# Kernel tuning notes

Hardware: AMD Instinct MI355X
Metric: run time of the kernel (lower is better)

## Reference

```python
import jax, jax.numpy as jnp
import numpy as np

NUM_NODES = 20000
HIDDEN = 64
NUM_EDGES = 640000
LEAK = 0.2  # PyG GATConv negative_slope default


def gat_conv(x, w, a_src, a_dst, b, src, dst, n):
    # x: [N, F_in]; w: [F_in, H*C]; a_src/a_dst: [H, C]; edges j=src -> i=dst
    H, C = a_src.shape
    xe = (x @ w).reshape(n, H, C)                         # [N, H, C]
    es = jnp.einsum('nhc,hc->nh', xe, a_src)              # alpha_src per node
    ed = jnp.einsum('nhc,hc->nh', xe, a_dst)              # alpha_dst per node
    e = jax.nn.leaky_relu(es[src] + ed[dst], LEAK)        # [E, H] edge logits
    # segment softmax over each destination's incoming edges
    m = jax.ops.segment_max(e, dst, num_segments=n)
    p = jnp.exp(e - m[dst])
    s = jax.ops.segment_sum(p, dst, num_segments=n)
    alpha = p / s[dst]                                    # [E, H]
    out = jax.ops.segment_sum(alpha[:, :, None] * xe[src], dst, num_segments=n)
    return out.reshape(n, H * C) + b                      # concat heads + bias


def setup_inputs() -> dict:
    key = jax.random.key(0)
    ks = jax.random.split(key, 16)
    B, S, N, Hd = 4, 12, NUM_NODES, HIDDEN
    sc = 0.1
    inp = {}
    inp['x'] = jax.random.normal(ks[0], (B, S, N), jnp.float32)
    inp['edge_index'] = jax.random.randint(ks[1], (2, NUM_EDGES), 0, N, jnp.int32)
    inp['proj_w'] = jax.random.normal(ks[2], (S, Hd), jnp.float32) * sc
    inp['proj_b'] = jnp.zeros((Hd,), jnp.float32)
    inp['gat0_w'] = jax.random.normal(ks[3], (Hd, Hd), jnp.float32) * sc
    inp['gat0_asrc'] = jax.random.normal(ks[4], (8, 8), jnp.float32) * sc
    inp['gat0_adst'] = jax.random.normal(ks[5], (8, 8), jnp.float32) * sc
    inp['gat0_b'] = jnp.zeros((Hd,), jnp.float32)
    inp['gat1_w'] = jax.random.normal(ks[6], (Hd, Hd), jnp.float32) * sc
    inp['gat1_asrc'] = jax.random.normal(ks[7], (8, 8), jnp.float32) * sc
    inp['gat1_adst'] = jax.random.normal(ks[8], (8, 8), jnp.float32) * sc
    inp['gat1_b'] = jnp.zeros((Hd,), jnp.float32)
    inp['gat2_w'] = jax.random.normal(ks[9], (Hd, Hd), jnp.float32) * sc
    inp['gat2_asrc'] = jax.random.normal(ks[10], (1, Hd), jnp.float32) * sc
    inp['gat2_adst'] = jax.random.normal(ks[11], (1, Hd), jnp.float32) * sc
    inp['gat2_b'] = jnp.zeros((Hd,), jnp.float32)
    inp['conv_w'] = jax.random.normal(ks[12], (Hd, Hd, 3), jnp.float32) * sc
    inp['conv_b'] = jnp.zeros((Hd,), jnp.float32)
    inp['out_w'] = jax.random.normal(ks[13], (Hd, 3), jnp.float32) * sc
    inp['out_b'] = jnp.zeros((3,), jnp.float32)
    return inp


def reference(x, edge_index, proj_w, proj_b,
              gat0_w, gat0_asrc, gat0_adst, gat0_b,
              gat1_w, gat1_asrc, gat1_adst, gat1_b,
              gat2_w, gat2_asrc, gat2_adst, gat2_b,
              conv_w, conv_b, out_w, out_b):
    B, S, N = x.shape
    # PyG GATConv add_self_loops=True
    loops = jnp.arange(N, dtype=edge_index.dtype)
    src = jnp.concatenate([edge_index[0], loops])
    dst = jnp.concatenate([edge_index[1], loops])
    h = jnp.transpose(x, (0, 2, 1)) @ proj_w + proj_b     # [B, N, Hd]
    layers = [(gat0_w, gat0_asrc, gat0_adst, gat0_b),
              (gat1_w, gat1_asrc, gat1_adst, gat1_b),
              (gat2_w, gat2_asrc, gat2_adst, gat2_b)]
    for i, (w, asr, ads, b) in enumerate(layers):
        h = jax.vmap(lambda hb: gat_conv(hb, w, asr, ads, b, src, dst, N))(h)
        if i < len(layers) - 1:
            h = jax.nn.elu(h)                             # dropout is identity in eval
    hc = jnp.transpose(h, (0, 2, 1))                      # [B, Hd, N]
    hc = jax.lax.conv_general_dilated(hc, conv_w, (1,), ((1, 1),),
                                      dimension_numbers=('NCH', 'OIH', 'NCH'))
    hc = jax.nn.relu(hc + conv_b[None, :, None])
    h = jnp.transpose(hc, (0, 2, 1)) @ out_w + out_b      # [B, N, pred]
    return jnp.transpose(h, (0, 2, 1))                    # [B, pred, N]
```

## Files before the change

### kernel.cpp

```cpp
#include <hip/hip_runtime.h>
#include <hip/hip_fp16.h>
#include <math.h>

constexpr int B  = 4;
constexpr int S  = 12;
constexpr int N  = 20000;
constexpr int HD = 64;
constexpr int E0 = 640000;
constexpr int EL = E0 + N;
constexpr int BN = B * N;
constexpr int CAP = 128;

__global__ void scatter_kernel(const int* __restrict__ ei, int* __restrict__ cnt,
                               int* __restrict__ perm) {
    int e = blockIdx.x * blockDim.x + threadIdx.x;
    if (e >= EL) return;
    int s, d;
    if (e < E0) { s = ei[e]; d = ei[E0 + e]; }
    else        { s = e - E0; d = s; }
    int pos = atomicAdd(&cnt[d], 1) & (CAP - 1);
    perm[d * CAP + pos] = s;
}

__global__ void tw_kernel(const float* __restrict__ cw, float* __restrict__ cwD) {
    int i = blockIdx.x * blockDim.x + threadIdx.x;
    if (i >= HD * HD * 3) return;
    int o = i / (HD * 3), rem = i % (HD * 3), c = rem / 3, dt = rem % 3;
    cwD[dt * (HD * HD) + c * HD + o] = cw[i];
}

constexpr int GT = 64;

template<int H>
__global__ __launch_bounds__(256, 4)
void gemm_attn_kernel(const float* __restrict__ hin, const float* __restrict__ w,
                      const float* __restrict__ asrc, const float* __restrict__ adst,
                      float* __restrict__ xe, float* __restrict__ es, float* __restrict__ ed) {
    __shared__ __half tileh[GT * HD];
    int base = blockIdx.x * GT;
    const float4* src4 = (const float4*)((const __half*)hin + (size_t)base * HD);
    for (int i = threadIdx.x; i < GT * HD / 8; i += 256)
        ((float4*)tileh)[i] = src4[i];
    int lane = threadIdx.x & 63;
    float wres[HD];
    #pragma unroll
    for (int c = 0; c < HD; ++c) wres[c] = w[c * HD + lane];
    float as_ = asrc[lane], ad_ = adst[lane];
    __syncthreads();
    int wvid = threadIdx.x >> 6;
    for (int j = wvid * 16; j < wvid * 16 + 16; ++j) {
        int t = base + j;
        float acc = 0.f;
        #pragma unroll
        for (int q = 0; q < 8; ++q) {
            float4 raw = ((const float4*)tileh)[j * 8 + q];
            const __half2* hp = (const __half2*)&raw;
            float2 v0 = __half22float2(hp[0]);
            float2 v1 = __half22float2(hp[1]);
            float2 v2 = __half22float2(hp[2]);
            float2 v3 = __half22float2(hp[3]);
            acc = fmaf(v0.x, wres[8*q+0], acc);
            acc = fmaf(v0.y, wres[8*q+1], acc);
            acc = fmaf(v1.x, wres[8*q+2], acc);
            acc = fmaf(v1.y, wres[8*q+3], acc);
            acc = fmaf(v2.x, wres[8*q+4], acc);
            acc = fmaf(v2.y, wres[8*q+5], acc);
            acc = fmaf(v3.x, wres[8*q+6], acc);
            acc = fmaf(v3.y, wres[8*q+7], acc);
        }
        ((__half*)xe)[(size_t)t * HD + lane] = __float2half(acc);
        float t0 = acc * as_, t1 = acc * ad_;
        if (H == 8) {
            #pragma unroll
            for (int m = 1; m < 8; m <<= 1) {
                t0 += __shfl_xor(t0, m, 64);
                t1 += __shfl_xor(t1, m, 64);
            }
            if ((lane & 7) == 0) {
                es[t * 8 + (lane >> 3)] = t0;
                ed[t * 8 + (lane >> 3)] = t1;
            }
        } else {
            #pragma unroll
            for (int m = 1; m < 64; m <<= 1) {
                t0 += __shfl_xor(t0, m, 64);
                t1 += __shfl_xor(t1, m, 64);
            }
            if (lane == 0) { es[t] = t0; ed[t] = t1; }
        }
    }
}

__global__ __launch_bounds__(256, 4)
void fused0_kernel(const float* __restrict__ x, const float* __restrict__ pw,
                   const float* __restrict__ pb, const float* __restrict__ w,
                   const float* __restrict__ asrc, const float* __restrict__ adst,
                   float* __restrict__ xe, float* __restrict__ es, float* __restrict__ ed) {
    __shared__ __half tileh[GT * HD];
    __shared__ float xt[S * GT];
    int base = blockIdx.x * GT;
    for (int i = threadIdx.x; i < S * GT; i += 256) {
        int s = i >> 6, nl = i & 63;
        int t = base + nl, bb = t / N, n = t - bb * N;
        xt[i] = x[(bb * S + s) * N + n];
    }
    int lane = threadIdx.x & 63;
    float wres[HD];
    #pragma unroll
    for (int c = 0; c < HD; ++c) wres[c] = w[c * HD + lane];
    float pwres[S];
    #pragma unroll
    for (int s = 0; s < S; ++s) pwres[s] = pw[s * HD + lane];
    float pbv = pb[lane];
    float as_ = asrc[lane], ad_ = adst[lane];
    __syncthreads();
    int wvid = threadIdx.x >> 6;
    for (int j = wvid * 16; j < wvid * 16 + 16; ++j) {
        float hl = pbv;
        #pragma unroll
        for (int s = 0; s < S; ++s)
            hl = fmaf(xt[s * GT + j], pwres[s], hl);
        tileh[j * HD + lane] = __float2half(hl);
    }
    for (int j = wvid * 16; j < wvid * 16 + 16; ++j) {
        int t = base + j;
        float acc = 0.f;
        #pragma unroll
        for (int q = 0; q < 8; ++q) {
            float4 raw = ((const float4*)tileh)[j * 8 + q];
            const __half2* hp = (const __half2*)&raw;
            float2 v0 = __half22float2(hp[0]);
            float2 v1 = __half22float2(hp[1]);
            float2 v2 = __half22float2(hp[2]);
            float2 v3 = __half22float2(hp[3]);
            acc = fmaf(v0.x, wres[8*q+0], acc);
            acc = fmaf(v0.y, wres[8*q+1], acc);
            acc = fmaf(v1.x, wres[8*q+2], acc);
            acc = fmaf(v1.y, wres[8*q+3], acc);
            acc = fmaf(v2.x, wres[8*q+4], acc);
            acc = fmaf(v2.y, wres[8*q+5], acc);
            acc = fmaf(v3.x, wres[8*q+6], acc);
            acc = fmaf(v3.y, wres[8*q+7], acc);
        }
        ((__half*)xe)[(size_t)t * HD + lane] = __float2half(acc);
        float t0 = acc * as_, t1 = acc * ad_;
        #pragma unroll
        for (int m = 1; m < 8; m <<= 1) {
            t0 += __shfl_xor(t0, m, 64);
            t1 += __shfl_xor(t1, m, 64);
        }
        if ((lane & 7) == 0) {
            es[t * 8 + (lane >> 3)] = t0;
            ed[t * 8 + (lane >> 3)] = t1;
        }
    }
}

template<int H, bool DO_ELU, bool OUT_HALF>
__global__ __launch_bounds__(256, 8)
void agg_kernel(const float* __restrict__ xe, const float* __restrict__ es,
                const float* __restrict__ ed, const int* __restrict__ cnt,
                const int* __restrict__ perm, const float* __restrict__ bias,
                float* __restrict__ hout) {
    int g = blockIdx.x;
    int bb   = (g & 7) >> 1;
    int idx  = (g >> 3) * 2 + (g & 1);
    int node = idx * 4 + (threadIdx.x >> 6);
    int lane  = threadIdx.x & 63;
    int group = lane >> 3;
    int c8    = lane & 7;
    int deg = cnt[node];
    int baseE = node * CAP;
    int h = (H == 8) ? c8 : 0;
    const float*  es_b = es + bb * (N * H);
    const __half* xeh  = (const __half*)xe + (size_t)bb * N * HD;
    float edv = ed[(bb * N + node) * H + h];
    float acc[8] = {0.f,0.f,0.f,0.f,0.f,0.f,0.f,0.f};
    float ssum = 0.f;
    #pragma unroll 4
    for (int jb = 0; jb < deg; jb += 8) {
        int j = jb + group;
        bool valid = (j < deg);
        int src = perm[baseE + (valid ? j : 0)];
        float e = es_b[src * H + h] + edv;
        e = fmaxf(e, 0.2f * e);
        float p = valid ? __expf(e) : 0.f;
        ssum += p;
        float4 raw = *(const float4*)(xeh + (size_t)src * HD + c8 * 8);
        const __half2* hp2 = (const __half2*)&raw;
        float2 v0 = __half22float2(hp2[0]);
        float2 v1 = __half22float2(hp2[1]);
        float2 v2 = __half22float2(hp2[2]);
        float2 v3 = __half22float2(hp2[3]);
        acc[0] = fmaf(p, v0.x, acc[0]);
        acc[1] = fmaf(p, v0.y, acc[1]);
        acc[2] = fmaf(p, v1.x, acc[2]);
        acc[3] = fmaf(p, v1.y, acc[3]);
        acc[4] = fmaf(p, v2.x, acc[4]);
        acc[5] = fmaf(p, v2.y, acc[5]);
        acc[6] = fmaf(p, v3.x, acc[6]);
        acc[7] = fmaf(p, v3.y, acc[7]);
    }
    #pragma unroll
    for (int m = 8; m < 64; m <<= 1) {
        #pragma unroll
        for (int k = 0; k < 8; ++k) acc[k] += __shfl_xor(acc[k], m, 64);
        ssum += __shfl_xor(ssum, m, 64);
    }
    if (lane < 8) {
        float inv = 1.f / ssum;
        const float4* b4 = (const float4*)bias;
        float4 b0 = b4[c8 * 2 + 0], b1 = b4[c8 * 2 + 1];
        float r[8];
        r[0] = acc[0] * inv + b0.x; r[1] = acc[1] * inv + b0.y;
        r[2] = acc[2] * inv + b0.z; r[3] = acc[3] * inv + b0.w;
        r[4] = acc[4] * inv + b1.x; r[5] = acc[5] * inv + b1.y;
        r[6] = acc[6] * inv + b1.z; r[7] = acc[7] * inv + b1.w;
        if (DO_ELU) {
            #pragma unroll
            for (int k = 0; k < 8; ++k)
                r[k] = (r[k] > 0.f) ? r[k] : expm1f(r[k]);
        }
        if (OUT_HALF) {
            union { __half2 h2[4]; float4 f4; } u;
            u.h2[0] = __floats2half2_rn(r[0], r[1]);
            u.h2[1] = __floats2half2_rn(r[2], r[3]);
            u.h2[2] = __floats2half2_rn(r[4], r[5]);
            u.h2[3] = __floats2half2_rn(r[6], r[7]);
            ((float4*)hout)[(size_t)(bb * N + node) * 8 + c8] = u.f4;
        } else {
            float4 lo = {r[0], r[1], r[2], r[3]};
            float4 hi = {r[4], r[5], r[6], r[7]};
            float4* o4 = (float4*)hout + (size_t)(bb * N + node) * 16 + c8 * 2;
            o4[0] = lo;
            o4[1] = hi;
        }
    }
}

constexpr int CVN = 16;
__global__ __launch_bounds__(128, 2)
void conv_out_kernel(const float* __restrict__ h, const float* __restrict__ cwD,
                     const float* __restrict__ cb, const float* __restrict__ ow,
                     const float* __restrict__ ob, float* __restrict__ out) {
    __shared__ float part[2 * CVN * HD];
    int bb = blockIdx.y;
    int wvid = __builtin_amdgcn_readfirstlane(threadIdx.x >> 6);
    int base = blockIdx.x * (2 * CVN) + wvid * CVN;
    int lane = threadIdx.x & 63;
    float* wp = part + wvid * (CVN * HD);
    const __half* hb = (const __half*)h;
    float cbv = cb[lane];
    float ow0 = ow[lane * 3 + 0], ow1 = ow[lane * 3 + 1], ow2 = ow[lane * 3 + 2];
    float ob0 = ob[0], ob1 = ob[1], ob2 = ob[2];
    #pragma unroll
    for (int j = 0; j < CVN; ++j) wp[j * HD + lane] = cbv;
    #pragma unroll 1
    for (int dt = 0; dt < 3; ++dt) {
        float wres[HD];
        #pragma unroll
        for (int c = 0; c < HD; ++c) wres[c] = cwD[dt * (HD * HD) + c * HD + lane];
        #pragma unroll 2
        for (int j = 0; j < CVN; ++j) {
            int m = base + j + dt - 1;
            if (m >= 0 && m < N) {
                const unsigned int* hpu =
                    (const unsigned int*)(hb + ((size_t)bb * N + m) * HD);
                float a = 0.f;
                #pragma unroll
                for (int c2 = 0; c2 < 32; ++c2) {
                    unsigned int wbits = hpu[c2];
                    __half2 h2 = *(const __half2*)&wbits;
                    float2 vf = __half22float2(h2);
                    a = fmaf(vf.x, wres[2 * c2 + 0], a);
                    a = fmaf(vf.y, wres[2 * c2 + 1], a);
                }
                wp[j * HD + lane] += a;
            }
        }
    }
    #pragma unroll 1
    for (int j = 0; j < CVN; ++j) {
        float v = fmaxf(wp[j * HD + lane], 0.f);
        float t0 = v * ow0, t1 = v * ow1, t2 = v * ow2;
        #pragma unroll
        for (int m = 1; m < 64; m <<= 1) {
            t0 += __shfl_xor(t0, m, 64);
            t1 += __shfl_xor(t1, m, 64);
            t2 += __shfl_xor(t2, m, 64);
        }
        int n = base + j;
        if (lane < 3) {
            float r = (lane == 0) ? t0 + ob0 : (lane == 1) ? t1 + ob1 : t2 + ob2;
            out[(size_t)bb * 3 * N + lane * N + n] = r;
        }
    }
}

extern "C" void kernel_launch(void* const* d_in, const int* in_sizes, int n_in,
                              void* d_out, int out_size, void* d_ws, size_t ws_size,
                              hipStream_t stream) {
    const float* x      = (const float*)d_in[0];
    const int*   ei     = (const int*)  d_in[1];
    const float* proj_w = (const float*)d_in[2];
    const float* proj_b = (const float*)d_in[3];
    const float* g_w [3] = {(const float*)d_in[4], (const float*)d_in[8],  (const float*)d_in[12]};
    const float* g_as[3] = {(const float*)d_in[5], (const float*)d_in[9],  (const float*)d_in[13]};
    const float* g_ad[3] = {(const float*)d_in[6], (const float*)d_in[10], (const float*)d_in[14]};
    const float* g_b [3] = {(const float*)d_in[7], (const float*)d_in[11], (const float*)d_in[15]};
    const float* conv_w = (const float*)d_in[16];
    const float* conv_b = (const float*)d_in[17];
    const float* out_w  = (const float*)d_in[18];
    const float* out_b  = (const float*)d_in[19];
    float* out = (float*)d_out;

    float* bufA = (float*)d_ws;
    float* bufX = bufA + (size_t)BN * HD;
    float* es   = bufX + (size_t)BN * HD;
    float* ed   = es   + (size_t)BN * 8;
    int* cnt  = (int*)(ed + (size_t)BN * 8);
    int* perm = cnt + N;
    float* cwD = (float*)(perm + (size_t)N * CAP);

    const int TB = 256;
    const int gE = (EL + TB - 1) / TB;

    hipMemsetAsync(cnt, 0, N * sizeof(int), stream);
    scatter_kernel<<<gE, TB, 0, stream>>>(ei, cnt, perm);

    tw_kernel<<<(HD * HD * 3 + TB - 1) / TB, TB, 0, stream>>>(conv_w, cwD);

    fused0_kernel<<<BN / GT, TB, 0, stream>>>(x, proj_w, proj_b, g_w[0], g_as[0], g_ad[0],
                                              bufX, es, ed);
    agg_kernel<8, true, true><<<BN / 4, TB, 0, stream>>>(bufX, es, ed, cnt, perm, g_b[0], bufA);

    gemm_attn_kernel<8><<<BN / GT, TB, 0, stream>>>(bufA, g_w[1], g_as[1], g_ad[1], bufX, es, ed);
    agg_kernel<8, true, true><<<BN / 4, TB, 0, stream>>>(bufX, es, ed, cnt, perm, g_b[1], bufA);

    gemm_attn_kernel<1><<<BN / GT, TB, 0, stream>>>(bufA, g_w[2], g_as[2], g_ad[2], bufX, es, ed);
    agg_kernel<1, false, true><<<BN / 4, TB, 0, stream>>>(bufX, es, ed, cnt, perm, g_b[2], bufA);

    conv_out_kernel<<<dim3(N / (2 * CVN), B), 128, 0, stream>>>(bufA, cwD, conv_b, out_w, out_b, out);
}
```

Before: 400.2 us.

## Restructure conv loop to load each input row once for all three taps

The temporal conv loop is reordered so each input row is loaded and converted from half once per channel half and reused for all three kernel taps, instead of being reloaded per tap. Weights for the three taps are held in registers split into two 32-channel chunks to keep register pressure similar. This cuts global loads of h roughly threefold in the conv_out kernel. In exchange the row loop is fully unrolled, which increases code size and may raise register use.

Result: no change. 403.0 us (+0.7%).

```diff
diff --git a/kernel.cpp b/kernel.cpp
--- a/kernel.cpp
+++ b/kernel.cpp
@@ -256,26 +256,47 @@
     #pragma unroll
     for (int j = 0; j < CVN; ++j) wp[j * HD + lane] = cbv;
     #pragma unroll 1
-    for (int dt = 0; dt < 3; ++dt) {
-        float wres[HD];
-        #pragma unroll
-        for (int c = 0; c < HD; ++c) wres[c] = cwD[dt * (HD * HD) + c * HD + lane];
-        #pragma unroll 2
-        for (int j = 0; j < CVN; ++j) {
-            int m = base + j + dt - 1;
+    for (int ch = 0; ch < 2; ++ch) {
+        float w0[32], w1[32], w2[32];
+        #pragma unroll
+        for (int c = 0; c < 32; ++c) {
+            w0[c] = cwD[0 * (HD * HD) + (ch * 32 + c) * HD + lane];
+            w1[c] = cwD[1 * (HD * HD) + (ch * 32 + c) * HD + lane];
+            w2[c] = cwD[2 * (HD * HD) + (ch * 32 + c) * HD + lane];
+        }
+        #pragma unroll
+        for (int rr = 0; rr < CVN + 2; ++rr) {
+            int m = base + rr - 1;
             if (m >= 0 && m < N) {
                 const unsigned int* hpu =
-                    (const unsigned int*)(hb + ((size_t)bb * N + m) * HD);
-                float a = 0.f;
+                    (const unsigned int*)(hb + ((size_t)bb * N + m) * HD + ch * 32);
+                float vf[32];
                 #pragma unroll
-                for (int c2 = 0; c2 < 32; ++c2) {
+                for (int c2 = 0; c2 < 16; ++c2) {
                     unsigned int wbits = hpu[c2];
                     __half2 h2 = *(const __half2*)&wbits;
-                    float2 vf = __half22float2(h2);
-                    a = fmaf(vf.x, wres[2 * c2 + 0], a);
-                    a = fmaf(vf.y, wres[2 * c2 + 1], a);
+                    float2 f = __half22float2(h2);
+                    vf[2 * c2 + 0] = f.x;
+                    vf[2 * c2 + 1] = f.y;
                 }
-                wp[j * HD + lane] += a;
+                if (rr <= CVN - 1) {
+                    float a = 0.f;
+                    #pragma unroll
+                    for (int c = 0; c < 32; ++c) a = fmaf(vf[c], w0[c], a);
+                    wp[rr * HD + lane] += a;
+                }
+                if (rr >= 1 && rr <= CVN) {
+                    float a = 0.f;
+                    #pragma unroll
+                    for (int c = 0; c < 32; ++c) a = fmaf(vf[c], w1[c], a);
+                    wp[(rr - 1) * HD + lane] += a;
+                }
+                if (rr >= 2) {
+                    float a = 0.f;
+                    #pragma unroll
+                    for (int c = 0; c < 32; ++c) a = fmaf(vf[c], w2[c], a);
+                    wp[(rr - 2) * HD + lane] += a;
+                }
             }
         }
     }
```
